# Kernel optimization log

Hardware: AMD Instinct MI355X
Metric: run time of the kernel (lower is better)

## Reference

```python
import jax, jax.numpy as jnp
import numpy as np

B, N, DIM = 4, 4096, 1024
HEADS, DIM_HEAD, BSZ, EPS = 8, 64, 16, 1e-8
INNER = HEADS * DIM_HEAD


def setup_inputs() -> dict:
    key = jax.random.key(0)
    k1, k2, k3 = jax.random.split(key, 3)
    x = jax.random.normal(k1, (B, N, DIM), dtype=jnp.float32)
    # torch nn.Linear weights are [out, in]; scale ~ fan_in^-0.5 for stable exp()
    w_qkv = jax.random.normal(k2, (3 * INNER, DIM), dtype=jnp.float32) * (DIM ** -0.5)
    w_out = jax.random.normal(k3, (DIM, INNER), dtype=jnp.float32) * (INNER ** -0.5)
    b_out = jnp.zeros((DIM,), dtype=jnp.float32)
    return {"x": x, "w_qkv": w_qkv, "w_out": w_out, "b_out": b_out}


def _to_bh(t, b, n):
    # 'b n (h d) -> (b h) n d'
    return t.reshape(b, n, HEADS, DIM_HEAD).transpose(0, 2, 1, 3).reshape(b * HEADS, n, DIM_HEAD)


def _to_blocks(t):
    # 'b (n z) d -> b n z d'
    return t.reshape(t.shape[0], -1, BSZ, DIM_HEAD)


def _calc_Y_and_A(qb, kb, vb):
    S = jnp.einsum('bnid,bnjd->bnij', qb, kb)   # block-local scores
    A = jnp.exp(S)
    y = jnp.einsum('bnij,bnjd->bnid', A, vb)
    return y.reshape(y.shape[0], -1, DIM_HEAD), A.sum(-1).reshape(A.shape[0], -1)


def _hattention(x, w_qkv, w_out, b_out):
    b, n, _ = x.shape
    qkv = x @ w_qkv.T
    q, k, v = jnp.split(qkv, 3, axis=-1)
    q, k, v = (_to_bh(t, b, n) for t in (q, k, v))
    q = q * (DIM_HEAD ** -0.5)

    num_levels = int(np.log2(n // BSZ)) - 1
    qkvs = [(q, k, v)]
    for _ in range(num_levels):
        q = q.reshape(q.shape[0], -1, 2, DIM_HEAD).mean(axis=2)
        k = k.reshape(k.shape[0], -1, 2, DIM_HEAD).mean(axis=2)
        v = v.reshape(v.shape[0], -1, 2, DIM_HEAD).sum(axis=2)
        qkvs.append((q, k, v))
    top_level = qkvs[0]
    coarse_levels = qkvs[1:][::-1]  # coarsest first

    Ys = []
    for (ql, kl, vl) in coarse_levels:
        qb, kb, vb = map(_to_blocks, (ql, kl, vl))
        bh, nb = kb.shape[0], kb.shape[1]
        # flip sibling key blocks: 'b (n r) z d' with r=2 reversed
        kb = kb.reshape(bh, nb // 2, 2, BSZ, DIM_HEAD)[:, :, ::-1].reshape(bh, nb, BSZ, DIM_HEAD)
        Ys.append(_calc_Y_and_A(qb, kb, vb))
    Ys.append(_calc_Y_and_A(*map(_to_blocks, top_level)))

    Y, A = Ys[0]
    for y_l, a_l in Ys[1:]:
        Y = jnp.repeat(Y, 2, axis=1) + y_l
        A = jnp.repeat(A, 2, axis=1) + a_l

    out = Y / (A + EPS)[..., None]
    # '(b h) n d -> b n (h d)'
    out = out.reshape(b, HEADS, n, DIM_HEAD).transpose(0, 2, 1, 3).reshape(b, n, INNER)
    return out @ w_out.T + b_out


def reference(x, w_qkv, w_out, b_out):
    return _hattention(x, w_qkv, w_out, b_out)
```

## Files before the change

### kernel.cpp

```cpp
#include <hip/hip_runtime.h>
#include <hip/hip_bf16.h>


typedef __bf16 bf16x8 __attribute__((ext_vector_type(8)));
typedef float floatx4 __attribute__((ext_vector_type(4)));
typedef unsigned short ushortx8 __attribute__((ext_vector_type(8)));
typedef unsigned int uintx4 __attribute__((ext_vector_type(4)));

#define ROWS_PER_BH 8160

__device__ __forceinline__ void g2lds16(const void* g, void* l) {
  __builtin_amdgcn_global_load_lds(
      (const __attribute__((address_space(1))) void*)g,
      (__attribute__((address_space(3))) void*)l, 16, 0, 0);
}

__device__ __forceinline__ unsigned short f2bu(float x) {
  __hip_bfloat16 h = __float2bfloat16(x);
  return *(unsigned short*)&h;
}
__device__ __forceinline__ float bu2f(unsigned short u) {
  __hip_bfloat16 h = *(__hip_bfloat16*)&u;
  return __bfloat162float(h);
}

__global__ __launch_bounds__(256) void f2b3_kernel(const float* __restrict__ x,
                                                   const float* __restrict__ wq,
                                                   const float* __restrict__ wo,
                                                   __hip_bfloat16* __restrict__ xb,
                                                   __hip_bfloat16* __restrict__ wqb,
                                                   __hip_bfloat16* __restrict__ wob) {
  int i0 = (blockIdx.x * 256 + threadIdx.x) * 4;
  const float* s;
  __hip_bfloat16* d;
  if (i0 < 16777216) {
    s = x; d = xb;
  } else if (i0 < 16777216 + 1572864) {
    s = wq + (i0 - 16777216); d = wqb + (i0 - 16777216);
    float4 v = *(const float4*)s;
    d[0] = __float2bfloat16(v.x); d[1] = __float2bfloat16(v.y);
    d[2] = __float2bfloat16(v.z); d[3] = __float2bfloat16(v.w);
    return;
  } else {
    s = wo + (i0 - 16777216 - 1572864); d = wob + (i0 - 16777216 - 1572864);
    float4 v = *(const float4*)s;
    d[0] = __float2bfloat16(v.x); d[1] = __float2bfloat16(v.y);
    d[2] = __float2bfloat16(v.z); d[3] = __float2bfloat16(v.w);
    return;
  }
  float4 v = *(const float4*)(s + i0);
  d[i0 + 0] = __float2bfloat16(v.x);
  d[i0 + 1] = __float2bfloat16(v.y);
  d[i0 + 2] = __float2bfloat16(v.z);
  d[i0 + 3] = __float2bfloat16(v.w);
}

template <int K>
__device__ __forceinline__ void gemm_core(const unsigned short* __restrict__ A,
                                          const unsigned short* __restrict__ B,
                                          unsigned short* ldsA, unsigned short* ldsB,
                                          int tM, int tN, floatx4 acc[4][4]) {
  const int tid = threadIdx.x;
  const int lane = tid & 63, w = tid >> 6;
  const int wm = w >> 1, wn = w & 1;
  const int lr = lane >> 3;
  const int gch = (lane & 7) ^ lr;
  const unsigned short* Ag = A + (size_t)(tM + w * 32 + lr) * K + gch * 8;
  const unsigned short* Bg = B + (size_t)(tN + w * 32 + lr) * K + gch * 8;
  unsigned short* lA = &ldsA[w * 2048 + lane * 8];
  unsigned short* lB = &ldsB[w * 2048 + lane * 8];

  const int rA = wm * 64 + (lane & 15);
  const int rB = wn * 64 + (lane & 15);
  const int quad = lane >> 4;
  const int sw = lane & 7;

  for (int kt = 0; kt < K; kt += 64) {
    __syncthreads();
#pragma unroll
    for (int c = 0; c < 4; c++) {
      g2lds16(Ag + (size_t)(c * 8) * K + kt, lA + c * 512);
      g2lds16(Bg + (size_t)(c * 8) * K + kt, lB + c * 512);
    }
    __syncthreads();
#pragma unroll
    for (int kk = 0; kk < 2; kk++) {
      bf16x8 af[4], bv[4];
#pragma unroll
      for (int i = 0; i < 4; i++)
        af[i] = *(const bf16x8*)&ldsA[(rA + i * 16) * 64 + (((kk * 4 + quad) ^ sw) * 8)];
#pragma unroll
      for (int j = 0; j < 4; j++)
        bv[j] = *(const bf16x8*)&ldsB[(rB + j * 16) * 64 + (((kk * 4 + quad) ^ sw) * 8)];
#pragma unroll
      for (int i = 0; i < 4; i++)
#pragma unroll
        for (int j = 0; j < 4; j++)
          acc[i][j] = __builtin_amdgcn_mfma_f32_16x16x32_bf16(af[i], bv[j], acc[i][j], 0, 0, 0);
    }
  }
}

__global__ __launch_bounds__(256) void gemm_qkv_kernel(
    const unsigned short* __restrict__ A,
    const unsigned short* __restrict__ B,
    __hip_bfloat16* __restrict__ qp, __hip_bfloat16* __restrict__ kp,
    __hip_bfloat16* __restrict__ vp) {
  __shared__ unsigned short ldsA[128 * 64];
  __shared__ unsigned short ldsB[128 * 64];
  const int lane = threadIdx.x & 63, w = threadIdx.x >> 6;
  const int wm = w >> 1, wn = w & 1;
  const int tM = blockIdx.x * 128, tN = blockIdx.y * 128;

  floatx4 acc[4][4];
#pragma unroll
  for (int i = 0; i < 4; i++)
#pragma unroll
    for (int j = 0; j < 4; j++) acc[i][j] = (floatx4){0.f, 0.f, 0.f, 0.f};

  gemm_core<1024>(A, B, ldsA, ldsB, tM, tN, acc);

  const int quad = lane >> 4, m15 = lane & 15;
#pragma unroll
  for (int i = 0; i < 4; i++) {
#pragma unroll
    for (int j = 0; j < 4; j++) {
      const int c = tN + wn * 64 + j * 16 + m15;
      const int tensor = c >> 9;
      const int rem = c & 511;
      const int h = rem >> 6, d = rem & 63;
      __hip_bfloat16* dstbuf = (tensor == 0) ? qp : ((tensor == 1) ? kp : vp);
      const float scale = (tensor == 0) ? 0.125f : 1.0f;
#pragma unroll
      for (int r = 0; r < 4; r++) {
        const int m = tM + wm * 64 + i * 16 + quad * 4 + r;
        const int b = m >> 12, n = m & 4095;
        size_t dst = ((size_t)(b * 8 + h) * ROWS_PER_BH + n) * 64 + d;
        dstbuf[dst] = __float2bfloat16(acc[i][j][r] * scale);
      }
      float s4 = acc[i][j][0] + acc[i][j][1] + acc[i][j][2] + acc[i][j][3];
      s4 += __shfl_xor(s4, 16, 64);
      s4 += __shfl_xor(s4, 32, 64);
      if (quad == 0) {
        const int mrow = tM + wm * 64 + i * 16;
        const int b = mrow >> 12, n4 = (mrow & 4095) >> 4;
        const float val = (tensor == 0) ? s4 * (0.125f / 16.f)
                         : ((tensor == 1) ? s4 * (1.f / 16.f) : s4);
        dstbuf[((size_t)(b * 8 + h) * ROWS_PER_BH + 7680 + n4) * 64 + d] =
            __float2bfloat16(val);
      }
    }
  }
}

__global__ __launch_bounds__(256) void gemm_out_kernel(
    const unsigned short* __restrict__ A,
    const unsigned short* __restrict__ B,
    const float* __restrict__ bias, float* __restrict__ out) {
  __shared__ unsigned short ldsA[128 * 64];
  __shared__ unsigned short ldsB[128 * 64];
  const int lane = threadIdx.x & 63, w = threadIdx.x >> 6;
  const int wm = w >> 1, wn = w & 1;
  const int tM = blockIdx.x * 128, tN = blockIdx.y * 128;

  floatx4 acc[4][4];
#pragma unroll
  for (int i = 0; i < 4; i++)
#pragma unroll
    for (int j = 0; j < 4; j++) acc[i][j] = (floatx4){0.f, 0.f, 0.f, 0.f};

  gemm_core<512>(A, B, ldsA, ldsB, tM, tN, acc);

  const int quad = lane >> 4;
#pragma unroll
  for (int i = 0; i < 4; i++) {
#pragma unroll
    for (int j = 0; j < 4; j++) {
      const int c = tN + wn * 64 + j * 16 + (lane & 15);
      const float bb = bias[c];
#pragma unroll
      for (int r = 0; r < 4; r++) {
        const int m = tM + wm * 64 + i * 16 + quad * 4 + r;
        out[(size_t)m * 1024 + c] = acc[i][j][r] + bb;
      }
    }
  }
}

__global__ __launch_bounds__(256) void pyramid47_kernel(
    __hip_bfloat16* __restrict__ qp, __hip_bfloat16* __restrict__ kp,
    __hip_bfloat16* __restrict__ vp) {
  __shared__ unsigned short qs[256 * 64], ks[256 * 64], vs[256 * 64];
  const int bh = blockIdx.x;
  const int tid = threadIdx.x;
  const size_t base = (size_t)bh * ROWS_PER_BH;
  const size_t g0 = (base + 7680) * 64;
  const unsigned short* qg = (const unsigned short*)qp;
  const unsigned short* kg = (const unsigned short*)kp;
  const unsigned short* vg = (const unsigned short*)vp;
#pragma unroll
  for (int c = 0; c < 8; c++) {
    int off = c * 2048 + tid * 8;
    *(ushortx8*)&qs[off] = *(const ushortx8*)(qg + g0 + off);
    *(ushortx8*)&ks[off] = *(const ushortx8*)(kg + g0 + off);
    *(ushortx8*)&vs[off] = *(const ushortx8*)(vg + g0 + off);
  }
  const int offs[4] = {0, 7936, 8064, 8128};
#pragma unroll
  for (int l = 1; l <= 3; l++) {
    __syncthreads();
    const int nOut = 256 >> l;
    for (int e = tid; e < nOut * 32; e += 256) {
      const int i = e >> 5, dp = (e & 31) * 2;
      const int a = (i << l) * 64 + dp;
      const int b = a + (1 << (l - 1)) * 64;
      unsigned short q0 = f2bu(0.5f * (bu2f(qs[a]) + bu2f(qs[b])));
      unsigned short q1 = f2bu(0.5f * (bu2f(qs[a + 1]) + bu2f(qs[b + 1])));
      unsigned short k0 = f2bu(0.5f * (bu2f(ks[a]) + bu2f(ks[b])));
      unsigned short k1 = f2bu(0.5f * (bu2f(ks[a + 1]) + bu2f(ks[b + 1])));
      unsigned short v0 = f2bu(bu2f(vs[a]) + bu2f(vs[b]));
      unsigned short v1 = f2bu(bu2f(vs[a + 1]) + bu2f(vs[b + 1]));
      qs[a] = q0; qs[a + 1] = q1;
      ks[a] = k0; ks[a + 1] = k1;
      vs[a] = v0; vs[a + 1] = v1;
      const size_t grow = (base + offs[l] + i) * 64 + dp;
      *(unsigned int*)((unsigned short*)qp + grow) = (unsigned int)q0 | ((unsigned int)q1 << 16);
      *(unsigned int*)((unsigned short*)kp + grow) = (unsigned int)k0 | ((unsigned int)k1 << 16);
      *(unsigned int*)((unsigned short*)vp + grow) = (unsigned int)v0 | ((unsigned int)v1 << 16);
    }
  }
}

__global__ __launch_bounds__(256) void attn47_kernel(
    const unsigned short* __restrict__ qp, const unsigned short* __restrict__ kp,
    const unsigned short* __restrict__ vp, __hip_bfloat16* __restrict__ yall,
    float* __restrict__ aall) {
  __shared__ __align__(16) unsigned short vT[4][64 * 24];
  const int w = threadIdx.x >> 6, lane = threadIdx.x & 63;
  const int g = blockIdx.x * 4 + w;
  if (g >= 30) return;
  const int bh = blockIdx.y;
  int level, blk;
  if (g < 16)      { level = 4; blk = g; }
  else if (g < 24) { level = 5; blk = g - 16; }
  else if (g < 28) { level = 6; blk = g - 24; }
  else             { level = 7; blk = g - 28; }
  const int ro = 8192 - (8192 >> level);
  const int kblk = blk ^ 1;
  const int m = lane & 15, q = lane >> 4;
  const size_t qbase = ((size_t)bh * ROWS_PER_BH + ro + blk * 16) * 64;
  const size_t kbase = ((size_t)bh * ROWS_PER_BH + ro + kblk * 16) * 64;

  const bf16x8 ka0 = *(const bf16x8*)(kp + kbase + m * 64 + q * 8);
  const bf16x8 ka1 = *(const bf16x8*)(kp + kbase + m * 64 + 32 + q * 8);
  const bf16x8 qb0 = *(const bf16x8*)(qp + qbase + m * 64 + q * 8);
  const bf16x8 qb1 = *(const bf16x8*)(qp + qbase + m * 64 + 32 + q * 8);

  const ushortx8 v0 = *(const ushortx8*)(vp + qbase + m * 64 + q * 16);
  const ushortx8 v1 = *(const ushortx8*)(vp + qbase + m * 64 + q * 16 + 8);
  unsigned short* vtw = vT[w];
#pragma unroll
  for (int j = 0; j < 8; j++) vtw[(q * 16 + j) * 24 + m] = v0[j];
#pragma unroll
  for (int j = 0; j < 8; j++) vtw[(q * 16 + 8 + j) * 24 + m] = v1[j];

  floatx4 s = (floatx4){0.f, 0.f, 0.f, 0.f};
  s = __builtin_amdgcn_mfma_f32_16x16x32_bf16(ka0, qb0, s, 0, 0, 0);
  s = __builtin_amdgcn_mfma_f32_16x16x32_bf16(ka1, qb1, s, 0, 0, 0);

  unsigned short pb0 = f2bu(__expf(s[0])), pb1 = f2bu(__expf(s[1]));
  unsigned short pb2 = f2bu(__expf(s[2])), pb3 = f2bu(__expf(s[3]));
  float asum = bu2f(pb0) + bu2f(pb1) + bu2f(pb2) + bu2f(pb3);
  asum += __shfl_xor(asum, 16, 64);
  asum += __shfl_xor(asum, 32, 64);
  const size_t arow = (size_t)bh * ROWS_PER_BH + ro + blk * 16;
  if (q == 0) aall[arow + m] = asum;

  unsigned int d0 = (unsigned int)pb0 | ((unsigned int)pb1 << 16);
  unsigned int d1 = (unsigned int)pb2 | ((unsigned int)pb3 << 16);
  const int s0l = m + 32 * (q & 1);
  unsigned int u0 = __shfl(d0, s0l, 64);
  unsigned int u1 = __shfl(d1, s0l, 64);
  unsigned int u2 = __shfl(d0, s0l + 16, 64);
  unsigned int u3 = __shfl(d1, s0l + 16, 64);
  union { uintx4 i; bf16x8 b; } pau;
  pau.i = (q < 2) ? (uintx4){u0, u1, u2, u3} : (uintx4){0u, 0u, 0u, 0u};
  const bf16x8 pa = pau.b;

#pragma unroll
  for (int c = 0; c < 4; c++) {
    union { uintx4 i; bf16x8 b; } bvu;
    bvu.i = (uintx4){0u, 0u, 0u, 0u};
    if (q < 2) bvu.b = *(const bf16x8*)&vtw[(c * 16 + m) * 24 + q * 8];
    floatx4 y = (floatx4){0.f, 0.f, 0.f, 0.f};
    y = __builtin_amdgcn_mfma_f32_16x16x32_bf16(pa, bvu.b, y, 0, 0, 0);
#pragma unroll
    for (int r = 0; r < 4; r++)
      yall[(arow + q * 4 + r) * 64 + c * 16 + m] = __float2bfloat16(y[r]);
  }
}

__global__ __launch_bounds__(256, 1) void fused03_kernel(
    const unsigned short* __restrict__ qp, const unsigned short* __restrict__ kp,
    const unsigned short* __restrict__ vp, const unsigned short* __restrict__ yall,
    const float* __restrict__ aall, __hip_bfloat16* __restrict__ Ub) {
  __shared__ __align__(16) unsigned short qs[256 * 64];
  __shared__ __align__(16) unsigned short ks[256 * 64];
  __shared__ __align__(16) unsigned short vs[256 * 64];
  __shared__ unsigned short ylds[224 * 72];
  __shared__ float alds[480];
  __shared__ __align__(16) unsigned short vT[4][64 * 24];

  const int tid = threadIdx.x;
  const int w = tid >> 6, lane = tid & 63;
  const int m = lane & 15, q = lane >> 4;
  const int c = blockIdx.x, bh = blockIdx.y;
  const size_t base = (size_t)bh * ROWS_PER_BH;
  const size_t g0 = (base + c * 256) * 64;

  auto sidx = [](int r, int d) {
    return r * 64 + (((d >> 3) ^ (r & 7)) << 3) + (d & 7);
  };
  unsigned short* vtw = vT[w];

  {
    const int srow = tid >> 3;
    const int sch = (tid & 7) ^ (srow & 7);
    const size_t gofs = (size_t)srow * 64 + sch * 8;
#pragma unroll
    for (int it = 0; it < 8; it++) {
      const size_t gi = g0 + (size_t)it * 2048 + gofs;
      g2lds16(qp + gi, &qs[it * 2048 + tid * 8]);
      g2lds16(kp + gi, &ks[it * 2048 + tid * 8]);
      g2lds16(vp + gi, &vs[it * 2048 + tid * 8]);
    }
  }
  __syncthreads();

  auto attn_block = [&](int level, int blk, bool flip, floatx4 yout[4]) -> float {
    const int kb = flip ? (blk ^ 1) : blk;
    const int Rq = (blk * 16 + m) << level;
    const int Rk = (kb * 16 + m) << level;
    const bf16x8 ka0 = *(const bf16x8*)&ks[sidx(Rk, q * 8)];
    const bf16x8 ka1 = *(const bf16x8*)&ks[sidx(Rk, 32 + q * 8)];
    const bf16x8 qb0 = *(const bf16x8*)&qs[sidx(Rq, q * 8)];
    const bf16x8 qb1 = *(const bf16x8*)&qs[sidx(Rq, 32 + q * 8)];
    const ushortx8 v0 = *(const ushortx8*)&vs[sidx(Rq, q * 16)];
    const ushortx8 v1 = *(const ushortx8*)&vs[sidx(Rq, q * 16 + 8)];
#pragma unroll
    for (int j = 0; j < 8; j++) vtw[(q * 16 + j) * 24 + m] = v0[j];
#pragma unroll
    for (int j = 0; j < 8; j++) vtw[(q * 16 + 8 + j) * 24 + m] = v1[j];

    floatx4 s = (floatx4){0.f, 0.f, 0.f, 0.f};
    s = __builtin_amdgcn_mfma_f32_16x16x32_bf16(ka0, qb0, s, 0, 0, 0);
    s = __builtin_amdgcn_mfma_f32_16x16x32_bf16(ka1, qb1, s, 0, 0, 0);

    unsigned short pb0 = f2bu(__expf(s[0])), pb1 = f2bu(__expf(s[1]));
    unsigned short pb2 = f2bu(__expf(s[2])), pb3 = f2bu(__expf(s[3]));
    float asum = bu2f(pb0) + bu2f(pb1) + bu2f(pb2) + bu2f(pb3);
    asum += __shfl_xor(asum, 16, 64);
    asum += __shfl_xor(asum, 32, 64);

    unsigned int d0 = (unsigned int)pb0 | ((unsigned int)pb1 << 16);
    unsigned int d1 = (unsigned int)pb2 | ((unsigned int)pb3 << 16);
    const int s0l = m + 32 * (q & 1);
    unsigned int u0 = __shfl(d0, s0l, 64);
    unsigned int u1 = __shfl(d1, s0l, 64);
    unsigned int u2 = __shfl(d0, s0l + 16, 64);
    unsigned int u3 = __shfl(d1, s0l + 16, 64);
    union { uintx4 i; bf16x8 b; } pau;
    pau.i = (q < 2) ? (uintx4){u0, u1, u2, u3} : (uintx4){0u, 0u, 0u, 0u};
    const bf16x8 pa = pau.b;

#pragma unroll
    for (int cc = 0; cc < 4; cc++) {
      union { uintx4 i; bf16x8 b; } bvu;
      bvu.i = (uintx4){0u, 0u, 0u, 0u};
      if (q < 2) bvu.b = *(const bf16x8*)&vtw[(cc * 16 + m) * 24 + q * 8];
      floatx4 y = (floatx4){0.f, 0.f, 0.f, 0.f};
      y = __builtin_amdgcn_mfma_f32_16x16x32_bf16(pa, bvu.b, y, 0, 0, 0);
      yout[cc] = y;
    }
    return asum;
  };

  auto pyr = [&](int l) {
    const int nOut = 256 >> l;
    for (int e = tid; e < nOut * 32; e += 256) {
      const int i = e >> 5, dp = (e & 31) * 2;
      const int ra = i << l, rb = ra + (1 << (l - 1));
      const int ia = sidx(ra, dp), ib = sidx(rb, dp);
      unsigned short q0 = f2bu(0.5f * (bu2f(qs[ia]) + bu2f(qs[ib])));
      unsigned short q1 = f2bu(0.5f * (bu2f(qs[ia + 1]) + bu2f(qs[ib + 1])));
      unsigned short k0 = f2bu(0.5f * (bu2f(ks[ia]) + bu2f(ks[ib])));
      unsigned short k1 = f2bu(0.5f * (bu2f(ks[ia + 1]) + bu2f(ks[ib + 1])));
      unsigned short v0 = f2bu(bu2f(vs[ia]) + bu2f(vs[ib]));
      unsigned short v1 = f2bu(bu2f(vs[ia + 1]) + bu2f(vs[ib + 1]));
      qs[ia] = q0; qs[ia + 1] = q1;
      ks[ia] = k0; ks[ia + 1] = k1;
      vs[ia] = v0; vs[ia + 1] = v1;
    }
  };

  floatx4 y0reg[4][4];
#pragma unroll
  for (int t = 0; t < 4; t++) {
    const int blk = w + t * 4;
    float a0 = attn_block(0, blk, false, y0reg[t]);
    if (q == 0) alds[224 + blk * 16 + m] = a0;
  }
  __syncthreads();

  pyr(1);
  __syncthreads();
  {
    floatx4 yt[4];
#pragma unroll
    for (int t = 0; t < 2; t++) {
      const int blk = w + t * 4;
      float a = attn_block(1, blk, true, yt);
      if (q == 0) alds[blk * 16 + m] = a;
#pragma unroll
      for (int cc = 0; cc < 4; cc++)
#pragma unroll
        for (int r = 0; r < 4; r++)
          ylds[(blk * 16 + q * 4 + r) * 72 + cc * 16 + m] = f2bu(yt[cc][r]);
    }
  }
  __syncthreads();
  pyr(2);
  __syncthreads();
  {
    floatx4 yt[4];
    const int blk = w;
    float a = attn_block(2, blk, true, yt);
    if (q == 0) alds[128 + blk * 16 + m] = a;
#pragma unroll
    for (int cc = 0; cc < 4; cc++)
#pragma unroll
      for (int r = 0; r < 4; r++)
        ylds[(128 + blk * 16 + q * 4 + r) * 72 + cc * 16 + m] = f2bu(yt[cc][r]);
  }
  __syncthreads();
  pyr(3);
  __syncthreads();
  if (w < 2) {
    floatx4 yt[4];
    const int blk = w;
    float a = attn_block(3, blk, true, yt);
    if (q == 0) alds[192 + blk * 16 + m] = a;
#pragma unroll
    for (int cc = 0; cc < 4; cc++)
#pragma unroll
      for (int r = 0; r < 4; r++)
        ylds[(192 + blk * 16 + q * 4 + r) * 72 + cc * 16 + m] = f2bu(yt[cc][r]);
  }
  __syncthreads();

  const int bO = bh >> 3, hO = bh & 7;
#pragma unroll
  for (int t = 0; t < 4; t++) {
    const int blk = w + t * 4;
    const int i4 = c * 16 + blk;
    const size_t r4 = base + 7680 + i4;
    const size_t r5 = base + 7936 + (i4 >> 1);
    const size_t r6 = base + 8064 + (i4 >> 2);
    const size_t r7 = base + 8128 + (i4 >> 3);
    const float acoarse = aall[r4] + aall[r5] + aall[r6] + aall[r7];

    float inv[4];
#pragma unroll
    for (int r = 0; r < 4; r++) {
      const int row = blk * 16 + q * 4 + r;
      const float atot = alds[224 + row] + alds[row >> 1] +
                         alds[128 + (row >> 2)] + alds[192 + (row >> 3)] +
                         acoarse + 1e-8f;
      inv[r] = 1.0f / atot;
    }

#pragma unroll
    for (int cc = 0; cc < 4; cc++) {
      const int col = cc * 16 + m;
      const float yc = bu2f(yall[r4 * 64 + col]) + bu2f(yall[r5 * 64 + col]) +
                       bu2f(yall[r6 * 64 + col]) + bu2f(yall[r7 * 64 + col]);
#pragma unroll
      for (int r = 0; r < 4; r++) {
        const int row = blk * 16 + q * 4 + r;
        const float num = y0reg[t][cc][r] + bu2f(ylds[(row >> 1) * 72 + col]) +
                          bu2f(ylds[(128 + (row >> 2)) * 72 + col]) +
                          bu2f(ylds[(192 + (row >> 3)) * 72 + col]) + yc;
        Ub[((size_t)bO * 4096 + c * 256 + row) * 512 + hO * 64 + col] =
            __float2bfloat16(num * inv[r]);
      }
    }
  }
}

extern "C" void kernel_launch(void* const* d_in, const int* in_sizes, int n_in,
                              void* d_out, int out_size, void* d_ws, size_t ws_size,
                              hipStream_t stream) {
  const float* x     = (const float*)d_in[0];
  const float* w_qkv = (const float*)d_in[1];
  const float* w_out = (const float*)d_in[2];
  const float* b_out = (const float*)d_in[3];
  float* out = (float*)d_out;

  char* ws = (char*)d_ws;
  __hip_bfloat16* xb    = (__hip_bfloat16*)(ws + 0);
  __hip_bfloat16* wqkvb = (__hip_bfloat16*)(ws + 33554432);
  __hip_bfloat16* wob   = (__hip_bfloat16*)(ws + 36700160);
  __hip_bfloat16* qp    = (__hip_bfloat16*)(ws + 37748736);
  __hip_bfloat16* kp    = (__hip_bfloat16*)(ws + 71172096);
  __hip_bfloat16* vp    = (__hip_bfloat16*)(ws + 104595456);
  __hip_bfloat16* yall  = (__hip_bfloat16*)(ws + 138018816);
  float* aall           = (float*)(ws + 171442176);
  __hip_bfloat16* Ub    = (__hip_bfloat16*)(ws + 172486656);

  f2b3_kernel<<<18432, 256, 0, stream>>>(x, w_qkv, w_out, xb, wqkvb, wob);

  gemm_qkv_kernel<<<dim3(128, 12), 256, 0, stream>>>(
      (const unsigned short*)xb, (const unsigned short*)wqkvb, qp, kp, vp);

  pyramid47_kernel<<<32, 256, 0, stream>>>(qp, kp, vp);

  attn47_kernel<<<dim3(8, 32), 256, 0, stream>>>(
      (const unsigned short*)qp, (const unsigned short*)kp,
      (const unsigned short*)vp, yall, aall);

  fused03_kernel<<<dim3(16, 32), 256, 0, stream>>>(
      (const unsigned short*)qp, (const unsigned short*)kp,
      (const unsigned short*)vp, (const unsigned short*)yall, aall, Ub);

  gemm_out_kernel<<<dim3(128, 8), 256, 0, stream>>>(
      (const unsigned short*)Ub, (const unsigned short*)wob, b_out, out);
}
```

Measured before the change: 262.9 us.

## Fuse coarse pyramid and level 4-7 attention into one kernel; use 512-thread blocks

Replaces the separate pyramid47 and attn47 kernels with a single coarse47 kernel. It loads the finest coarse level into LDS, builds levels 5-7 in place, and computes the block attention per level without writing pyramid rows back to global memory. The fused03 kernel moves from 256 to 512 threads per block, so each wave handles fewer blocks. This removes one launch and a global round-trip, but the coarse kernel runs only 32 blocks and idles waves at the deeper levels.

```diff
diff --git a/kernel.cpp b/kernel.cpp
--- a/kernel.cpp
+++ b/kernel.cpp
@@ -187,136 +187,21 @@
   }
 }
 
-__global__ __launch_bounds__(256) void pyramid47_kernel(
-    __hip_bfloat16* __restrict__ qp, __hip_bfloat16* __restrict__ kp,
-    __hip_bfloat16* __restrict__ vp) {
-  __shared__ unsigned short qs[256 * 64], ks[256 * 64], vs[256 * 64];
-  const int bh = blockIdx.x;
-  const int tid = threadIdx.x;
-  const size_t base = (size_t)bh * ROWS_PER_BH;
-  const size_t g0 = (base + 7680) * 64;
-  const unsigned short* qg = (const unsigned short*)qp;
-  const unsigned short* kg = (const unsigned short*)kp;
-  const unsigned short* vg = (const unsigned short*)vp;
-#pragma unroll
-  for (int c = 0; c < 8; c++) {
-    int off = c * 2048 + tid * 8;
-    *(ushortx8*)&qs[off] = *(const ushortx8*)(qg + g0 + off);
-    *(ushortx8*)&ks[off] = *(const ushortx8*)(kg + g0 + off);
-    *(ushortx8*)&vs[off] = *(const ushortx8*)(vg + g0 + off);
-  }
-  const int offs[4] = {0, 7936, 8064, 8128};
-#pragma unroll
-  for (int l = 1; l <= 3; l++) {
-    __syncthreads();
-    const int nOut = 256 >> l;
-    for (int e = tid; e < nOut * 32; e += 256) {
-      const int i = e >> 5, dp = (e & 31) * 2;
-      const int a = (i << l) * 64 + dp;
-      const int b = a + (1 << (l - 1)) * 64;
-      unsigned short q0 = f2bu(0.5f * (bu2f(qs[a]) + bu2f(qs[b])));
-      unsigned short q1 = f2bu(0.5f * (bu2f(qs[a + 1]) + bu2f(qs[b + 1])));
-      unsigned short k0 = f2bu(0.5f * (bu2f(ks[a]) + bu2f(ks[b])));
-      unsigned short k1 = f2bu(0.5f * (bu2f(ks[a + 1]) + bu2f(ks[b + 1])));
-      unsigned short v0 = f2bu(bu2f(vs[a]) + bu2f(vs[b]));
-      unsigned short v1 = f2bu(bu2f(vs[a + 1]) + bu2f(vs[b + 1]));
-      qs[a] = q0; qs[a + 1] = q1;
-      ks[a] = k0; ks[a + 1] = k1;
-      vs[a] = v0; vs[a + 1] = v1;
-      const size_t grow = (base + offs[l] + i) * 64 + dp;
-      *(unsigned int*)((unsigned short*)qp + grow) = (unsigned int)q0 | ((unsigned int)q1 << 16);
-      *(unsigned int*)((unsigned short*)kp + grow) = (unsigned int)k0 | ((unsigned int)k1 << 16);
-      *(unsigned int*)((unsigned short*)vp + grow) = (unsigned int)v0 | ((unsigned int)v1 << 16);
-    }
-  }
-}
-
-__global__ __launch_bounds__(256) void attn47_kernel(
+__global__ __launch_bounds__(512, 1) void coarse47_kernel(
     const unsigned short* __restrict__ qp, const unsigned short* __restrict__ kp,
     const unsigned short* __restrict__ vp, __hip_bfloat16* __restrict__ yall,
     float* __restrict__ aall) {
-  __shared__ __align__(16) unsigned short vT[4][64 * 24];
-  const int w = threadIdx.x >> 6, lane = threadIdx.x & 63;
-  const int g = blockIdx.x * 4 + w;
-  if (g >= 30) return;
-  const int bh = blockIdx.y;
-  int level, blk;
-  if (g < 16)      { level = 4; blk = g; }
-  else if (g < 24) { level = 5; blk = g - 16; }
-  else if (g < 28) { level = 6; blk = g - 24; }
-  else             { level = 7; blk = g - 28; }
-  const int ro = 8192 - (8192 >> level);
-  const int kblk = blk ^ 1;
-  const int m = lane & 15, q = lane >> 4;
-  const size_t qbase = ((size_t)bh * ROWS_PER_BH + ro + blk * 16) * 64;
-  const size_t kbase = ((size_t)bh * ROWS_PER_BH + ro + kblk * 16) * 64;
-
-  const bf16x8 ka0 = *(const bf16x8*)(kp + kbase + m * 64 + q * 8);
-  const bf16x8 ka1 = *(const bf16x8*)(kp + kbase + m * 64 + 32 + q * 8);
-  const bf16x8 qb0 = *(const bf16x8*)(qp + qbase + m * 64 + q * 8);
-  const bf16x8 qb1 = *(const bf16x8*)(qp + qbase + m * 64 + 32 + q * 8);
-
-  const ushortx8 v0 = *(const ushortx8*)(vp + qbase + m * 64 + q * 16);
-  const ushortx8 v1 = *(const ushortx8*)(vp + qbase + m * 64 + q * 16 + 8);
-  unsigned short* vtw = vT[w];
-#pragma unroll
-  for (int j = 0; j < 8; j++) vtw[(q * 16 + j) * 24 + m] = v0[j];
-#pragma unroll
-  for (int j = 0; j < 8; j++) vtw[(q * 16 + 8 + j) * 24 + m] = v1[j];
-
-  floatx4 s = (floatx4){0.f, 0.f, 0.f, 0.f};
-  s = __builtin_amdgcn_mfma_f32_16x16x32_bf16(ka0, qb0, s, 0, 0, 0);
-  s = __builtin_amdgcn_mfma_f32_16x16x32_bf16(ka1, qb1, s, 0, 0, 0);
-
-  unsigned short pb0 = f2bu(__expf(s[0])), pb1 = f2bu(__expf(s[1]));
-  unsigned short pb2 = f2bu(__expf(s[2])), pb3 = f2bu(__expf(s[3]));
-  float asum = bu2f(pb0) + bu2f(pb1) + bu2f(pb2) + bu2f(pb3);
-  asum += __shfl_xor(asum, 16, 64);
-  asum += __shfl_xor(asum, 32, 64);
-  const size_t arow = (size_t)bh * ROWS_PER_BH + ro + blk * 16;
-  if (q == 0) aall[arow + m] = asum;
-
-  unsigned int d0 = (unsigned int)pb0 | ((unsigned int)pb1 << 16);
-  unsigned int d1 = (unsigned int)pb2 | ((unsigned int)pb3 << 16);
-  const int s0l = m + 32 * (q & 1);
-  unsigned int u0 = __shfl(d0, s0l, 64);
-  unsigned int u1 = __shfl(d1, s0l, 64);
-  unsigned int u2 = __shfl(d0, s0l + 16, 64);
-  unsigned int u3 = __shfl(d1, s0l + 16, 64);
-  union { uintx4 i; bf16x8 b; } pau;
-  pau.i = (q < 2) ? (uintx4){u0, u1, u2, u3} : (uintx4){0u, 0u, 0u, 0u};
-  const bf16x8 pa = pau.b;
-
-#pragma unroll
-  for (int c = 0; c < 4; c++) {
-    union { uintx4 i; bf16x8 b; } bvu;
-    bvu.i = (uintx4){0u, 0u, 0u, 0u};
-    if (q < 2) bvu.b = *(const bf16x8*)&vtw[(c * 16 + m) * 24 + q * 8];
-    floatx4 y = (floatx4){0.f, 0.f, 0.f, 0.f};
-    y = __builtin_amdgcn_mfma_f32_16x16x32_bf16(pa, bvu.b, y, 0, 0, 0);
-#pragma unroll
-    for (int r = 0; r < 4; r++)
-      yall[(arow + q * 4 + r) * 64 + c * 16 + m] = __float2bfloat16(y[r]);
-  }
-}
-
-__global__ __launch_bounds__(256, 1) void fused03_kernel(
-    const unsigned short* __restrict__ qp, const unsigned short* __restrict__ kp,
-    const unsigned short* __restrict__ vp, const unsigned short* __restrict__ yall,
-    const float* __restrict__ aall, __hip_bfloat16* __restrict__ Ub) {
   __shared__ __align__(16) unsigned short qs[256 * 64];
   __shared__ __align__(16) unsigned short ks[256 * 64];
   __shared__ __align__(16) unsigned short vs[256 * 64];
-  __shared__ unsigned short ylds[224 * 72];
-  __shared__ float alds[480];
-  __shared__ __align__(16) unsigned short vT[4][64 * 24];
+  __shared__ __align__(16) unsigned short vT[8][64 * 24];
 
   const int tid = threadIdx.x;
   const int w = tid >> 6, lane = tid & 63;
   const int m = lane & 15, q = lane >> 4;
-  const int c = blockIdx.x, bh = blockIdx.y;
+  const int bh = blockIdx.x;
   const size_t base = (size_t)bh * ROWS_PER_BH;
-  const size_t g0 = (base + c * 256) * 64;
+  const size_t g0 = (base + 7680) * 64;
 
   auto sidx = [](int r, int d) {
     return r * 64 + (((d >> 3) ^ (r & 7)) << 3) + (d & 7);
@@ -328,11 +213,11 @@
     const int sch = (tid & 7) ^ (srow & 7);
     const size_t gofs = (size_t)srow * 64 + sch * 8;
 #pragma unroll
-    for (int it = 0; it < 8; it++) {
-      const size_t gi = g0 + (size_t)it * 2048 + gofs;
-      g2lds16(qp + gi, &qs[it * 2048 + tid * 8]);
-      g2lds16(kp + gi, &ks[it * 2048 + tid * 8]);
-      g2lds16(vp + gi, &vs[it * 2048 + tid * 8]);
+    for (int it = 0; it < 4; it++) {
+      const size_t gi = g0 + (size_t)it * 4096 + gofs;
+      g2lds16(qp + gi, &qs[it * 4096 + tid * 8]);
+      g2lds16(kp + gi, &ks[it * 4096 + tid * 8]);
+      g2lds16(vp + gi, &vs[it * 4096 + tid * 8]);
     }
   }
   __syncthreads();
@@ -387,7 +272,7 @@
 
   auto pyr = [&](int l) {
     const int nOut = 256 >> l;
-    for (int e = tid; e < nOut * 32; e += 256) {
+    for (int e = tid; e < nOut * 32; e += 512) {
       const int i = e >> 5, dp = (e & 31) * 2;
       const int ra = i << l, rb = ra + (1 << (l - 1));
       const int ia = sidx(ra, dp), ib = sidx(rb, dp);
@@ -403,10 +288,158 @@
     }
   };
 
-  floatx4 y0reg[4][4];
-#pragma unroll
-  for (int t = 0; t < 4; t++) {
-    const int blk = w + t * 4;
+  auto emit = [&](int ro, int blk, const floatx4 yt[4], float a) {
+    const size_t arow = base + ro + blk * 16;
+    if (q == 0) aall[arow + m] = a;
+#pragma unroll
+    for (int cc = 0; cc < 4; cc++)
+#pragma unroll
+      for (int r = 0; r < 4; r++)
+        yall[(arow + q * 4 + r) * 64 + cc * 16 + m] = __float2bfloat16(yt[cc][r]);
+  };
+
+  {
+    floatx4 yt[4];
+#pragma unroll
+    for (int t = 0; t < 2; t++) {
+      const int blk = w + t * 8;
+      float a = attn_block(0, blk, true, yt);
+      emit(7680, blk, yt, a);
+    }
+  }
+  __syncthreads();
+  pyr(1);
+  __syncthreads();
+  {
+    floatx4 yt[4];
+    float a = attn_block(1, w, true, yt);
+    emit(7936, w, yt, a);
+  }
+  __syncthreads();
+  pyr(2);
+  __syncthreads();
+  if (w < 4) {
+    floatx4 yt[4];
+    float a = attn_block(2, w, true, yt);
+    emit(8064, w, yt, a);
+  }
+  __syncthreads();
+  pyr(3);
+  __syncthreads();
+  if (w < 2) {
+    floatx4 yt[4];
+    float a = attn_block(3, w, true, yt);
+    emit(8128, w, yt, a);
+  }
+}
+
+__global__ __launch_bounds__(512, 1) void fused03_kernel(
+    const unsigned short* __restrict__ qp, const unsigned short* __restrict__ kp,
+    const unsigned short* __restrict__ vp, const unsigned short* __restrict__ yall,
+    const float* __restrict__ aall, __hip_bfloat16* __restrict__ Ub) {
+  __shared__ __align__(16) unsigned short qs[256 * 64];
+  __shared__ __align__(16) unsigned short ks[256 * 64];
+  __shared__ __align__(16) unsigned short vs[256 * 64];
+  __shared__ unsigned short ylds[224 * 72];
+  __shared__ float alds[480];
+  __shared__ __align__(16) unsigned short vT[8][64 * 24];
+
+  const int tid = threadIdx.x;
+  const int w = tid >> 6, lane = tid & 63;
+  const int m = lane & 15, q = lane >> 4;
+  const int c = blockIdx.x, bh = blockIdx.y;
+  const size_t base = (size_t)bh * ROWS_PER_BH;
+  const size_t g0 = (base + c * 256) * 64;
+
+  auto sidx = [](int r, int d) {
+    return r * 64 + (((d >> 3) ^ (r & 7)) << 3) + (d & 7);
+  };
+  unsigned short* vtw = vT[w];
+
+  {
+    const int srow = tid >> 3;
+    const int sch = (tid & 7) ^ (srow & 7);
+    const size_t gofs = (size_t)srow * 64 + sch * 8;
+#pragma unroll
+    for (int it = 0; it < 4; it++) {
+      const size_t gi = g0 + (size_t)it * 4096 + gofs;
+      g2lds16(qp + gi, &qs[it * 4096 + tid * 8]);
+      g2lds16(kp + gi, &ks[it * 4096 + tid * 8]);
+      g2lds16(vp + gi, &vs[it * 4096 + tid * 8]);
+    }
+  }
+  __syncthreads();
+
+  auto attn_block = [&](int level, int blk, bool flip, floatx4 yout[4]) -> float {
+    const int kb = flip ? (blk ^ 1) : blk;
+    const int Rq = (blk * 16 + m) << level;
+    const int Rk = (kb * 16 + m) << level;
+    const bf16x8 ka0 = *(const bf16x8*)&ks[sidx(Rk, q * 8)];
+    const bf16x8 ka1 = *(const bf16x8*)&ks[sidx(Rk, 32 + q * 8)];
+    const bf16x8 qb0 = *(const bf16x8*)&qs[sidx(Rq, q * 8)];
+    const bf16x8 qb1 = *(const bf16x8*)&qs[sidx(Rq, 32 + q * 8)];
+    const ushortx8 v0 = *(const ushortx8*)&vs[sidx(Rq, q * 16)];
+    const ushortx8 v1 = *(const ushortx8*)&vs[sidx(Rq, q * 16 + 8)];
+#pragma unroll
+    for (int j = 0; j < 8; j++) vtw[(q * 16 + j) * 24 + m] = v0[j];
+#pragma unroll
+    for (int j = 0; j < 8; j++) vtw[(q * 16 + 8 + j) * 24 + m] = v1[j];
+
+    floatx4 s = (floatx4){0.f, 0.f, 0.f, 0.f};
+    s = __builtin_amdgcn_mfma_f32_16x16x32_bf16(ka0, qb0, s, 0, 0, 0);
+    s = __builtin_amdgcn_mfma_f32_16x16x32_bf16(ka1, qb1, s, 0, 0, 0);
+
+    unsigned short pb0 = f2bu(__expf(s[0])), pb1 = f2bu(__expf(s[1]));
+    unsigned short pb2 = f2bu(__expf(s[2])), pb3 = f2bu(__expf(s[3]));
+    float asum = bu2f(pb0) + bu2f(pb1) + bu2f(pb2) + bu2f(pb3);
+    asum += __shfl_xor(asum, 16, 64);
+    asum += __shfl_xor(asum, 32, 64);
+
+    unsigned int d0 = (unsigned int)pb0 | ((unsigned int)pb1 << 16);
+    unsigned int d1 = (unsigned int)pb2 | ((unsigned int)pb3 << 16);
+    const int s0l = m + 32 * (q & 1);
+    unsigned int u0 = __shfl(d0, s0l, 64);
+    unsigned int u1 = __shfl(d1, s0l, 64);
+    unsigned int u2 = __shfl(d0, s0l + 16, 64);
+    unsigned int u3 = __shfl(d1, s0l + 16, 64);
+    union { uintx4 i; bf16x8 b; } pau;
+    pau.i = (q < 2) ? (uintx4){u0, u1, u2, u3} : (uintx4){0u, 0u, 0u, 0u};
+    const bf16x8 pa = pau.b;
+
+#pragma unroll
+    for (int cc = 0; cc < 4; cc++) {
+      union { uintx4 i; bf16x8 b; } bvu;
+      bvu.i = (uintx4){0u, 0u, 0u, 0u};
+      if (q < 2) bvu.b = *(const bf16x8*)&vtw[(cc * 16 + m) * 24 + q * 8];
+      floatx4 y = (floatx4){0.f, 0.f, 0.f, 0.f};
+      y = __builtin_amdgcn_mfma_f32_16x16x32_bf16(pa, bvu.b, y, 0, 0, 0);
+      yout[cc] = y;
+    }
+    return asum;
+  };
+
+  auto pyr = [&](int l) {
+    const int nOut = 256 >> l;
+    for (int e = tid; e < nOut * 32; e += 512) {
+      const int i = e >> 5, dp = (e & 31) * 2;
+      const int ra = i << l, rb = ra + (1 << (l - 1));
+      const int ia = sidx(ra, dp), ib = sidx(rb, dp);
+      unsigned short q0 = f2bu(0.5f * (bu2f(qs[ia]) + bu2f(qs[ib])));
+      unsigned short q1 = f2bu(0.5f * (bu2f(qs[ia + 1]) + bu2f(qs[ib + 1])));
+      unsigned short k0 = f2bu(0.5f * (bu2f(ks[ia]) + bu2f(ks[ib])));
+      unsigned short k1 = f2bu(0.5f * (bu2f(ks[ia + 1]) + bu2f(ks[ib + 1])));
+      unsigned short v0 = f2bu(bu2f(vs[ia]) + bu2f(vs[ib]));
+      unsigned short v1 = f2bu(bu2f(vs[ia + 1]) + bu2f(vs[ib + 1]));
+      qs[ia] = q0; qs[ia + 1] = q1;
+      ks[ia] = k0; ks[ia + 1] = k1;
+      vs[ia] = v0; vs[ia + 1] = v1;
+    }
+  };
+
+  floatx4 y0reg[2][4];
+#pragma unroll
+  for (int t = 0; t < 2; t++) {
+    const int blk = w + t * 8;
     float a0 = attn_block(0, blk, false, y0reg[t]);
     if (q == 0) alds[224 + blk * 16 + m] = a0;
   }
@@ -416,22 +449,19 @@
   __syncthreads();
   {
     floatx4 yt[4];
-#pragma unroll
-    for (int t = 0; t < 2; t++) {
-      const int blk = w + t * 4;
-      float a = attn_block(1, blk, true, yt);
-      if (q == 0) alds[blk * 16 + m] = a;
-#pragma unroll
-      for (int cc = 0; cc < 4; cc++)
-#pragma unroll
-        for (int r = 0; r < 4; r++)
-          ylds[(blk * 16 + q * 4 + r) * 72 + cc * 16 + m] = f2bu(yt[cc][r]);
-    }
+    const int blk = w;
+    float a = attn_block(1, blk, true, yt);
+    if (q == 0) alds[blk * 16 + m] = a;
+#pragma unroll
+    for (int cc = 0; cc < 4; cc++)
+#pragma unroll
+      for (int r = 0; r < 4; r++)
+        ylds[(blk * 16 + q * 4 + r) * 72 + cc * 16 + m] = f2bu(yt[cc][r]);
   }
   __syncthreads();
   pyr(2);
   __syncthreads();
-  {
+  if (w < 4) {
     floatx4 yt[4];
     const int blk = w;
     float a = attn_block(2, blk, true, yt);
@@ -460,8 +490,8 @@
 
   const int bO = bh >> 3, hO = bh & 7;
 #pragma unroll
-  for (int t = 0; t < 4; t++) {
-    const int blk = w + t * 4;
+  for (int t = 0; t < 2; t++) {
+    const int blk = w + t * 8;
     const int i4 = c * 16 + blk;
     const size_t r4 = base + 7680 + i4;
     const size_t r5 = base + 7936 + (i4 >> 1);
@@ -522,13 +552,11 @@
   gemm_qkv_kernel<<<dim3(128, 12), 256, 0, stream>>>(
       (const unsigned short*)xb, (const unsigned short*)wqkvb, qp, kp, vp);
 
-  pyramid47_kernel<<<32, 256, 0, stream>>>(qp, kp, vp);
-
-  attn47_kernel<<<dim3(8, 32), 256, 0, stream>>>(
+  coarse47_kernel<<<32, 512, 0, stream>>>(
       (const unsigned short*)qp, (const unsigned short*)kp,
       (const unsigned short*)vp, yall, aall);
 
-  fused03_kernel<<<dim3(16, 32), 256, 0, stream>>>(
+  fused03_kernel<<<dim3(16, 32), 512, 0, stream>>>(
       (const unsigned short*)qp, (const unsigned short*)kp,
       (const unsigned short*)vp, (const unsigned short*)yall, aall, Ub);
 
```

Measured after the change: 247.1 us. 1.06x faster.
